# Kernel optimization log

Hardware: AMD Instinct MI355X
Metric: run time of the kernel (lower is better)

Reference implementation:

```python
import jax, jax.numpy as jnp
import numpy as np

B, T, C = 4, 2048, 1024
E, I, K = 8, 1408, 2
N_SHARED = 1
IS = I * N_SHARED  # shared expert intermediate size


def setup_inputs() -> dict:
    key = jax.random.key(0)
    ks = jax.random.split(key, 8)
    s = 0.02
    return {
        "x": jax.random.normal(ks[0], (B, T, C), dtype=jnp.float32),
        "Wg": jax.random.normal(ks[1], (E, C), dtype=jnp.float32) * s,   # gate: Linear(C->E), weight [out,in]
        "W1": jax.random.normal(ks[2], (E, I, C), dtype=jnp.float32) * s,  # fc_1 per expert
        "W2": jax.random.normal(ks[3], (E, I, C), dtype=jnp.float32) * s,  # fc_2 per expert
        "W3": jax.random.normal(ks[4], (E, C, I), dtype=jnp.float32) * s,  # proj per expert
        "Ws1": jax.random.normal(ks[5], (IS, C), dtype=jnp.float32) * s,   # shared expert fc_1
        "Ws2": jax.random.normal(ks[6], (IS, C), dtype=jnp.float32) * s,   # shared expert fc_2
        "Ws3": jax.random.normal(ks[7], (C, IS), dtype=jnp.float32) * s,   # shared expert proj
    }


def reference(x, Wg, W1, W2, W3, Ws1, Ws2, Ws3):
    b, t, c = x.shape
    xf = x.reshape(-1, c)                       # [N, C]
    n = xf.shape[0]

    # Router: softmax in float32, top-k gating
    logits = xf @ Wg.T                          # [N, E]
    probs = jax.nn.softmax(logits.astype(jnp.float32), axis=-1)
    topk_p, topk_i = jax.lax.top_k(probs, K)    # [N, K]
    topk_p = topk_p.astype(x.dtype)

    # Dense combine weights: w[n, e] = sum_k topk_p[n, k] * (topk_i[n, k] == e)
    comb = jnp.zeros((n, E), dtype=x.dtype).at[jnp.arange(n)[:, None], topk_i].add(topk_p)

    # All experts on all tokens (dense equivalent of masked dispatch), weighted combine
    g = jnp.einsum('nc,eic->nei', xf, W1)       # [N, E, I]
    u = jnp.einsum('nc,eic->nei', xf, W2)       # [N, E, I]
    h = jax.nn.silu(g) * u                      # SwiGLU
    o = jnp.einsum('nei,eci->nec', h, W3)       # [N, E, C]
    y = jnp.einsum('nec,ne->nc', o, comb).reshape(b, t, c)

    # Shared expert on the residual input
    shared = (jax.nn.silu(x @ Ws1.T) * (x @ Ws2.T)) @ Ws3.T  # [B, T, C]
    return y + shared
```

## Files before the change

kernel.cpp:

```cpp
#include <hip/hip_runtime.h>
#include <stdint.h>

typedef __bf16 bf16;
typedef __attribute__((ext_vector_type(8))) __bf16 bf16x8;
typedef __attribute__((ext_vector_type(4))) float f32x4;

#define N_TOK 8192
#define C_DIM 1024
#define I_DIM 1408
#define NE 8
#define NEA 9
#define H_ROWS 25600

#define CNT_OFF   0
#define OFFS_OFF  64
#define TT_OFF    128
#define BTOK_OFF  192
#define BP_OFF    (BTOK_OFF + NE * N_TOK * 4)
#define ROUTER_END (BP_OFF + NE * N_TOK * 4)
#define TSEL_OFF  ROUTER_END
#define TP0_OFF   (TSEL_OFF + N_TOK * 4)
#define TP1_OFF   (TP0_OFF + N_TOK * 4)
#define XB_OFF    (1u << 20)
#define WB1_OFF   (18u << 20)
#define WB2_OFF   (43u << 20)
#define WB3_OFF   (68u << 20)
#define H_OFF     (93u << 20)

__device__ __forceinline__ void gload16(const void* g, void* l) {
  __builtin_amdgcn_global_load_lds(
      (const __attribute__((address_space(1))) void*)g,
      (__attribute__((address_space(3))) void*)l, 16, 0, 0);
}

#define SCHED() __builtin_amdgcn_sched_barrier(0)
#define BAR()   __builtin_amdgcn_s_barrier()
#define VM4()   asm volatile("s_waitcnt vmcnt(4)" ::: "memory")
#define VM0()   asm volatile("s_waitcnt vmcnt(0)" ::: "memory")

#define MM(AV, BV, H)                                                          \
  {                                                                            \
    __builtin_amdgcn_s_setprio(1);                                             \
    _Pragma("unroll") for (int q = 0; q < 4; ++q)                              \
        _Pragma("unroll") for (int nf = 0; nf < 4; ++nf)                       \
            acc[(H)*4 + q][nf] = __builtin_amdgcn_mfma_f32_16x16x32_bf16(      \
                AV[q], BV[nf], acc[(H)*4 + q][nf], 0, 0, 0);                   \
    __builtin_amdgcn_s_setprio(0);                                             \
  }

__global__ __launch_bounds__(256) void convert_kernel(
    const float* __restrict__ src, bf16* __restrict__ dst, int n8) {
  int i = blockIdx.x * 256 + threadIdx.x;
  if (i >= n8) return;
  const float* s = src + (size_t)i * 8;
  float4 a = *(const float4*)(s);
  float4 b = *(const float4*)(s + 4);
  bf16x8 v;
  v[0] = (bf16)a.x; v[1] = (bf16)a.y; v[2] = (bf16)a.z; v[3] = (bf16)a.w;
  v[4] = (bf16)b.x; v[5] = (bf16)b.y; v[6] = (bf16)b.z; v[7] = (bf16)b.w;
  *(bf16x8*)(dst + (size_t)i * 8) = v;
}

__global__ __launch_bounds__(256) void logits_kernel(
    const float* __restrict__ x, const float* __restrict__ Wg,
    int* __restrict__ tsel, float* __restrict__ tp0, float* __restrict__ tp1) {
  __shared__ __align__(16) float wg[NE * C_DIM];
  int t = threadIdx.x;
#pragma unroll
  for (int j = 0; j < 8; ++j) {
    int idx = (t + 256 * j) * 4;
    *(float4*)&wg[idx] = *(const float4*)&Wg[idx];
  }
  __syncthreads();
  int wid = t >> 6, lane = t & 63;
  int tok = blockIdx.x * 4 + wid;
  const float* xr = x + (size_t)tok * C_DIM;
  float acc[NE];
#pragma unroll
  for (int e = 0; e < NE; ++e) acc[e] = 0.f;
#pragma unroll
  for (int j = 0; j < 4; ++j) {
    int c4 = (lane + 64 * j) * 4;
    float4 xv = *(const float4*)&xr[c4];
#pragma unroll
    for (int e = 0; e < NE; ++e) {
      float4 wv = *(const float4*)&wg[e * C_DIM + c4];
      acc[e] += xv.x * wv.x + xv.y * wv.y + xv.z * wv.z + xv.w * wv.w;
    }
  }
  for (int o = 32; o >= 1; o >>= 1)
#pragma unroll
    for (int e = 0; e < NE; ++e) acc[e] += __shfl_xor(acc[e], o, 64);
  if (lane == 0) {
    float m = acc[0];
#pragma unroll
    for (int e = 1; e < NE; ++e) m = fmaxf(m, acc[e]);
    float p[NE], s = 0.f;
#pragma unroll
    for (int e = 0; e < NE; ++e) { p[e] = __expf(acc[e] - m); s += p[e]; }
    float inv = 1.f / s;
#pragma unroll
    for (int e = 0; e < NE; ++e) p[e] *= inv;
    int e0 = 0; float p0 = p[0];
#pragma unroll
    for (int e = 1; e < NE; ++e) if (p[e] > p0) { p0 = p[e]; e0 = e; }
    int e1 = -1; float p1 = -1.f;
#pragma unroll
    for (int e = 0; e < NE; ++e) {
      if (e == e0) continue;
      if (p[e] > p1) { p1 = p[e]; e1 = e; }
    }
    tsel[tok] = e0 | (e1 << 8);
    tp0[tok] = p0;
    tp1[tok] = p1;
  }
}

__global__ __launch_bounds__(1024) void bucketize_kernel(
    const int* __restrict__ tsel, const float* __restrict__ tp0,
    const float* __restrict__ tp1, int* __restrict__ cnt,
    int* __restrict__ btok, float* __restrict__ bp) {
  int e = blockIdx.x;
  int t = threadIdx.x;
  __shared__ int psum[1024];
  int sel[8], loc[8];
  int cntloc = 0;
  int base_tok = t * 8;
#pragma unroll
  for (int j = 0; j < 8; ++j) {
    int s = tsel[base_tok + j];
    int hit = ((s & 0xff) == e) ? 1 : ((((s >> 8) & 0xff) == e) ? 2 : 0);
    sel[j] = hit;
    loc[j] = cntloc;
    cntloc += (hit != 0);
  }
  psum[t] = cntloc;
  __syncthreads();
  for (int off = 1; off < 1024; off <<= 1) {
    int v = (t >= off) ? psum[t - off] : 0;
    __syncthreads();
    psum[t] += v;
    __syncthreads();
  }
  int excl = psum[t] - cntloc;
  if (t == 1023) cnt[e] = psum[1023];
#pragma unroll
  for (int j = 0; j < 8; ++j) {
    if (sel[j]) {
      int pos = excl + loc[j];
      int tok = base_tok + j;
      btok[e * N_TOK + pos] = tok;
      bp[e * N_TOK + pos] = (sel[j] == 1) ? tp0[tok] : tp1[tok];
    }
  }
}

__global__ void offsets_kernel(const int* __restrict__ cnt, int* __restrict__ offs,
                               int* __restrict__ tt) {
  if (threadIdx.x == 0) {
    int a = 0, b = 0;
    for (int e = 0; e < NE; ++e) {
      offs[e] = a; tt[e] = b;
      int pad = (cnt[e] + 127) & ~127;
      a += pad;
      b += (pad + 255) >> 8;
    }
    offs[NE] = a; tt[NE] = b;
  }
}

__device__ __forceinline__ int swz_off(int row, int kg) {
  return row * 64 + ((kg ^ ((row >> 1) & 3)) * 16);
}

__global__ __launch_bounds__(512) void stage1_kernel(
    const bf16* __restrict__ xb, const bf16* __restrict__ wb1,
    const bf16* __restrict__ wb2, const int* __restrict__ cnt,
    const int* __restrict__ offs, const int* __restrict__ tt,
    const int* __restrict__ btok, bf16* __restrict__ H) {
  int bid = blockIdx.x;
  int wgid = (bid & 7) * 154 + (bid >> 3);
  int tau = wgid % 112;
  int i0 = (wgid / 112) * 128;
  int e, row0, slotbase, limit;
  if (tau < 32) {
    e = NE; row0 = tau * 256; slotbase = 0; limit = N_TOK;
  } else {
    int tr = tau - 32;
    if (tr >= tt[NE]) return;
    e = NE - 1;
#pragma unroll
    for (int q = 0; q < NE; ++q) if (tr < tt[q + 1]) { e = q; break; }
    row0 = (tr - tt[e]) * 256;
    slotbase = N_TOK + offs[e];
    limit = cnt[e];
    if (row0 >= limit) return;
  }

  __shared__ __align__(16) char smem[131072];
  const int t = threadIdx.x;
  const int lane = t & 63, wid = t >> 6;
  const int wr = wid >> 2, wc = wid & 3;
  const int l15 = lane & 15, l4 = lane >> 4;

  const int srow = t >> 2;
  const int gsrc = (t & 3) ^ ((srow >> 1) & 3);
  int ar0 = row0 + srow, ar1 = row0 + srow + 128;
  int tok0, tok1;
  if (e == NE) { tok0 = ar0; tok1 = ar1; }
  else {
    int ix0 = e * N_TOK + (ar0 < N_TOK ? ar0 : N_TOK - 1);
    int ix1 = e * N_TOK + (ar1 < N_TOK ? ar1 : N_TOK - 1);
    tok0 = btok[ix0] & (N_TOK - 1);
    tok1 = btok[ix1] & (N_TOK - 1);
  }
  const bf16* asrc0 = xb + (size_t)tok0 * C_DIM + gsrc * 8;
  const bf16* asrc1 = xb + (size_t)tok1 * C_DIM + gsrc * 8;
  const bf16* bsrc0;
  const bf16* bsrc1;
  {
    int r = srow;
    int q = r >> 4, m = q >> 1, sel = q & 1;
    int irow = i0 + m * 16 + (r & 15);
    bsrc0 = (sel ? wb2 : wb1) + ((size_t)e * I_DIM + irow) * C_DIM + gsrc * 8;
    r = srow + 128;
    q = r >> 4; m = q >> 1; sel = q & 1;
    irow = i0 + m * 16 + (r & 15);
    bsrc1 = (sel ? wb2 : wb1) + ((size_t)e * I_DIM + irow) * C_DIM + gsrc * 8;
  }
  const int lo0 = t * 16;
  const int NKT = C_DIM / 32;

  auto stAB = [&](int z) {
    if (z < NKT) {
      char* d = smem + (z & 3) * 32768;
      int k = z * 32;
      gload16(bsrc0 + k, d + 16384 + lo0);
      gload16(bsrc1 + k, d + 24576 + lo0);
      gload16(asrc0 + k, d + lo0);
      gload16(asrc1 + k, d + 8192 + lo0);
    }
  };

  int aoff[8], boff[4];
#pragma unroll
  for (int mf = 0; mf < 8; ++mf) aoff[mf] = swz_off(wr * 128 + mf * 16 + l15, l4);
#pragma unroll
  for (int nf = 0; nf < 4; ++nf) boff[nf] = swz_off(wc * 64 + nf * 16 + l15, l4);

  f32x4 acc[8][4];
  f32x4 zero = {0.f, 0.f, 0.f, 0.f};
#pragma unroll
  for (int mf = 0; mf < 8; ++mf)
#pragma unroll
    for (int nf = 0; nf < 4; ++nf) acc[mf][nf] = zero;

  bf16x8 av0[4], av1[4], bvA[4], bvB[4];
  auto rdA = [&](bf16x8* dst, int T, int h) {
    char* base = smem + (T & 3) * 32768;
#pragma unroll
    for (int q = 0; q < 4; ++q) dst[q] = *(const bf16x8*)(base + aoff[h * 4 + q]);
  };
  auto rdB = [&](bf16x8* dst, int T) {
    char* base = smem + (T & 3) * 32768 + 16384;
#pragma unroll
    for (int nf = 0; nf < 4; ++nf) dst[nf] = *(const bf16x8*)(base + boff[nf]);
  };

  stAB(0); stAB(1); stAB(2);
  SCHED(); VM4(); BAR(); SCHED();
  rdA(av0, 0, 0); rdB(bvA, 0);

  const int NIT = NKT / 2;
  for (int it = 0; it < NIT; ++it) {
    int z0 = 2 * it, z1 = 2 * it + 1;
    stAB(z0 + 3);
    rdA(av1, z0, 1);
    MM(av0, bvA, 0);
    rdA(av0, z1, 0); rdB(bvB, z1);
    MM(av1, bvA, 1);
    SCHED(); VM4(); BAR(); SCHED();
    stAB(z1 + 3);
    rdA(av1, z1, 1);
    MM(av0, bvB, 0);
    if (z1 + 1 < NKT) { rdA(av0, z1 + 1, 0); rdB(bvA, z1 + 1); }
    MM(av1, bvB, 1);
    SCHED(); VM4(); BAR(); SCHED();
  }
  VM0();

#pragma unroll
  for (int mf = 0; mf < 8; ++mf)
#pragma unroll
    for (int r = 0; r < 4; ++r) {
      int rr = row0 + wr * 128 + mf * 16 + l4 * 4 + r;
      if (rr < limit) {
#pragma unroll
        for (int p = 0; p < 2; ++p) {
          float g = acc[mf][2 * p][r];
          float u = acc[mf][2 * p + 1][r];
          float h = (g / (1.f + __expf(-g))) * u;
          int col = i0 + (wc * 2 + p) * 16 + l15;
          H[(size_t)(slotbase + rr) * I_DIM + col] = (bf16)h;
        }
      }
    }
}

template <int SHARED>
__global__ __launch_bounds__(512) void stage2_kernel(
    const bf16* __restrict__ H, const bf16* __restrict__ wb3,
    const int* __restrict__ cnt, const int* __restrict__ offs,
    const int* __restrict__ tt, const int* __restrict__ btok,
    const float* __restrict__ bp, float* __restrict__ y) {
  int bid = blockIdx.x;
  int e, row0, slotbase, limit, c0;
  if (SHARED) {
    int wgid = (bid & 7) * 16 + (bid >> 3);
    e = NE; row0 = (wgid % 32) * 256; slotbase = 0; limit = N_TOK;
    c0 = (wgid / 32) * 256;
  } else {
    int wgid = (bid & 7) * 40 + (bid >> 3);
    int tr = wgid % 80;
    c0 = (wgid / 80) * 256;
    if (tr >= tt[NE]) return;
    e = NE - 1;
#pragma unroll
    for (int q = 0; q < NE; ++q) if (tr < tt[q + 1]) { e = q; break; }
    row0 = (tr - tt[e]) * 256;
    slotbase = N_TOK + offs[e];
    limit = cnt[e];
    if (row0 >= limit) return;
  }

  __shared__ __align__(16) char smem[131072];
  const int t = threadIdx.x;
  const int lane = t & 63, wid = t >> 6;
  const int wr = wid >> 2, wc = wid & 3;
  const int l15 = lane & 15, l4 = lane >> 4;

  const int srow = t >> 2;
  const int gsrc = (t & 3) ^ ((srow >> 1) & 3);
  int sr0 = slotbase + row0 + srow;        if (sr0 > H_ROWS - 1) sr0 = H_ROWS - 1;
  int sr1 = slotbase + row0 + srow + 128;  if (sr1 > H_ROWS - 1) sr1 = H_ROWS - 1;
  const bf16* asrc0 = H + (size_t)sr0 * I_DIM + gsrc * 8;
  const bf16* asrc1 = H + (size_t)sr1 * I_DIM + gsrc * 8;
  const bf16* bsrc0 = wb3 + ((size_t)e * C_DIM + c0 + srow) * I_DIM + gsrc * 8;
  const bf16* bsrc1 = bsrc0 + (size_t)128 * I_DIM;
  const int lo0 = t * 16;
  const int NKT = I_DIM / 32;

  auto stAB = [&](int z) {
    if (z < NKT) {
      char* d = smem + (z & 3) * 32768;
      int k = z * 32;
      gload16(bsrc0 + k, d + 16384 + lo0);
      gload16(bsrc1 + k, d + 24576 + lo0);
      gload16(asrc0 + k, d + lo0);
      gload16(asrc1 + k, d + 8192 + lo0);
    }
  };

  int aoff[8], boff[4];
#pragma unroll
  for (int mf = 0; mf < 8; ++mf) aoff[mf] = swz_off(wr * 128 + mf * 16 + l15, l4);
#pragma unroll
  for (int nf = 0; nf < 4; ++nf) boff[nf] = swz_off(wc * 64 + nf * 16 + l15, l4);

  f32x4 acc[8][4];
  f32x4 zero = {0.f, 0.f, 0.f, 0.f};
#pragma unroll
  for (int mf = 0; mf < 8; ++mf)
#pragma unroll
    for (int nf = 0; nf < 4; ++nf) acc[mf][nf] = zero;

  bf16x8 av0[4], av1[4], bvA[4], bvB[4];
  auto rdA = [&](bf16x8* dst, int T, int h) {
    char* base = smem + (T & 3) * 32768;
#pragma unroll
    for (int q = 0; q < 4; ++q) dst[q] = *(const bf16x8*)(base + aoff[h * 4 + q]);
  };
  auto rdB = [&](bf16x8* dst, int T) {
    char* base = smem + (T & 3) * 32768 + 16384;
#pragma unroll
    for (int nf = 0; nf < 4; ++nf) dst[nf] = *(const bf16x8*)(base + boff[nf]);
  };

  stAB(0); stAB(1); stAB(2);
  SCHED(); VM4(); BAR(); SCHED();
  rdA(av0, 0, 0); rdB(bvA, 0);

  const int NIT = NKT / 2;
  for (int it = 0; it < NIT; ++it) {
    int z0 = 2 * it, z1 = 2 * it + 1;
    stAB(z0 + 3);
    rdA(av1, z0, 1);
    MM(av0, bvA, 0);
    rdA(av0, z1, 0); rdB(bvB, z1);
    MM(av1, bvA, 1);
    SCHED(); VM4(); BAR(); SCHED();
    stAB(z1 + 3);
    rdA(av1, z1, 1);
    MM(av0, bvB, 0);
    if (z1 + 1 < NKT) { rdA(av0, z1 + 1, 0); rdB(bvA, z1 + 1); }
    MM(av1, bvB, 1);
    SCHED(); VM4(); BAR(); SCHED();
  }
  VM0();

#pragma unroll
  for (int mf = 0; mf < 8; ++mf)
#pragma unroll
    for (int r = 0; r < 4; ++r) {
      int idx = row0 + wr * 128 + mf * 16 + l4 * 4 + r;
      if (idx < limit) {
        if (SHARED) {
#pragma unroll
          for (int nf = 0; nf < 4; ++nf) {
            int col = c0 + wc * 64 + nf * 16 + l15;
            y[(size_t)idx * C_DIM + col] = acc[mf][nf][r];
          }
        } else {
          float p = bp[e * N_TOK + idx];
          int tok = btok[e * N_TOK + idx] & (N_TOK - 1);
#pragma unroll
          for (int nf = 0; nf < 4; ++nf) {
            int col = c0 + wc * 64 + nf * 16 + l15;
            atomicAdd(&y[(size_t)tok * C_DIM + col], p * acc[mf][nf][r]);
          }
        }
      }
    }
}

extern "C" void kernel_launch(void* const* d_in, const int* in_sizes, int n_in,
                              void* d_out, int out_size, void* d_ws, size_t ws_size,
                              hipStream_t stream) {
  const float* x = (const float*)d_in[0];
  const float* Wg = (const float*)d_in[1];
  const float* W1 = (const float*)d_in[2];
  const float* W2 = (const float*)d_in[3];
  const float* W3 = (const float*)d_in[4];
  const float* Ws1 = (const float*)d_in[5];
  const float* Ws2 = (const float*)d_in[6];
  const float* Ws3 = (const float*)d_in[7];
  float* y = (float*)d_out;
  char* ws = (char*)d_ws;

  int* cnt = (int*)(ws + CNT_OFF);
  int* offs = (int*)(ws + OFFS_OFF);
  int* tt = (int*)(ws + TT_OFF);
  int* btok = (int*)(ws + BTOK_OFF);
  float* bp = (float*)(ws + BP_OFF);
  int* tsel = (int*)(ws + TSEL_OFF);
  float* tp0 = (float*)(ws + TP0_OFF);
  float* tp1 = (float*)(ws + TP1_OFF);
  bf16* xb = (bf16*)(ws + XB_OFF);
  bf16* wb1 = (bf16*)(ws + WB1_OFF);
  bf16* wb2 = (bf16*)(ws + WB2_OFF);
  bf16* wb3 = (bf16*)(ws + WB3_OFF);
  bf16* H = (bf16*)(ws + H_OFF);

  hipMemsetAsync(ws, 0, ROUTER_END, stream);

  auto conv = [&](const float* s, bf16* d, size_t n) {
    int n8 = (int)(n / 8);
    convert_kernel<<<(n8 + 255) / 256, 256, 0, stream>>>(s, d, n8);
  };
  conv(x, xb, (size_t)N_TOK * C_DIM);
  conv(W1, wb1, (size_t)NE * I_DIM * C_DIM);
  conv(Ws1, wb1 + (size_t)NE * I_DIM * C_DIM, (size_t)I_DIM * C_DIM);
  conv(W2, wb2, (size_t)NE * I_DIM * C_DIM);
  conv(Ws2, wb2 + (size_t)NE * I_DIM * C_DIM, (size_t)I_DIM * C_DIM);
  conv(W3, wb3, (size_t)NE * C_DIM * I_DIM);
  conv(Ws3, wb3 + (size_t)NE * C_DIM * I_DIM, (size_t)C_DIM * I_DIM);

  logits_kernel<<<N_TOK / 4, 256, 0, stream>>>(x, Wg, tsel, tp0, tp1);
  bucketize_kernel<<<NE, 1024, 0, stream>>>(tsel, tp0, tp1, cnt, btok, bp);
  offsets_kernel<<<1, 64, 0, stream>>>(cnt, offs, tt);

  stage1_kernel<<<1232, 512, 0, stream>>>(xb, wb1, wb2, cnt, offs, tt, btok, H);
  stage2_kernel<1><<<128, 512, 0, stream>>>(H, wb3, cnt, offs, tt, btok, bp, y);
  stage2_kernel<0><<<320, 512, 0, stream>>>(H, wb3, cnt, offs, tt, btok, bp, y);
}
```

Measured before the change: 407.4 us.

## Shrink GEMM tiles to 128x128 with 256-thread blocks and simple double buffering

Both grouped-GEMM stages move from 256x256 tiles with 512 threads and a 4-stage LDS ring to 128x128 tiles with 256 threads and a 2-stage buffer. The K loop is simplified to load, compute, then wait for all loads and barrier. Routed-expert padding granularity drops to 128 rows, which cuts wasted rows and raises block count and occupancy (launch bounds of 4 blocks). The cost is lower data reuse per tile, more global/L2 traffic, and less latency hiding from a full vmcnt(0) wait every iteration.

Measured after the change: 410.7 us. About the same (+0.8%).

```diff
diff --git a/kernel.cpp b/kernel.cpp
--- a/kernel.cpp
+++ b/kernel.cpp
@@ -35,18 +35,7 @@
 
 #define SCHED() __builtin_amdgcn_sched_barrier(0)
 #define BAR()   __builtin_amdgcn_s_barrier()
-#define VM4()   asm volatile("s_waitcnt vmcnt(4)" ::: "memory")
 #define VM0()   asm volatile("s_waitcnt vmcnt(0)" ::: "memory")
-
-#define MM(AV, BV, H)                                                          \
-  {                                                                            \
-    __builtin_amdgcn_s_setprio(1);                                             \
-    _Pragma("unroll") for (int q = 0; q < 4; ++q)                              \
-        _Pragma("unroll") for (int nf = 0; nf < 4; ++nf)                       \
-            acc[(H)*4 + q][nf] = __builtin_amdgcn_mfma_f32_16x16x32_bf16(      \
-                AV[q], BV[nf], acc[(H)*4 + q][nf], 0, 0, 0);                   \
-    __builtin_amdgcn_s_setprio(0);                                             \
-  }
 
 __global__ __launch_bounds__(256) void convert_kernel(
     const float* __restrict__ src, bf16* __restrict__ dst, int n8) {
@@ -163,7 +152,7 @@
       offs[e] = a; tt[e] = b;
       int pad = (cnt[e] + 127) & ~127;
       a += pad;
-      b += (pad + 255) >> 8;
+      b += pad >> 7;
     }
     offs[NE] = a; tt[NE] = b;
   }
@@ -173,39 +162,42 @@
   return row * 64 + ((kg ^ ((row >> 1) & 3)) * 16);
 }
 
-__global__ __launch_bounds__(512) void stage1_kernel(
+#define ROUTED_MAX 136
+#define TAU1 (64 + ROUTED_MAX)
+
+__global__ __launch_bounds__(256, 4) void stage1_kernel(
     const bf16* __restrict__ xb, const bf16* __restrict__ wb1,
     const bf16* __restrict__ wb2, const int* __restrict__ cnt,
     const int* __restrict__ offs, const int* __restrict__ tt,
     const int* __restrict__ btok, bf16* __restrict__ H) {
   int bid = blockIdx.x;
-  int wgid = (bid & 7) * 154 + (bid >> 3);
-  int tau = wgid % 112;
-  int i0 = (wgid / 112) * 128;
+  int wgid = (bid & 7) * 550 + (bid >> 3);
+  int tau = wgid % TAU1;
+  int i0 = (wgid / TAU1) * 64;
   int e, row0, slotbase, limit;
-  if (tau < 32) {
-    e = NE; row0 = tau * 256; slotbase = 0; limit = N_TOK;
+  if (tau < 64) {
+    e = NE; row0 = tau * 128; slotbase = 0; limit = N_TOK;
   } else {
-    int tr = tau - 32;
+    int tr = tau - 64;
     if (tr >= tt[NE]) return;
     e = NE - 1;
 #pragma unroll
     for (int q = 0; q < NE; ++q) if (tr < tt[q + 1]) { e = q; break; }
-    row0 = (tr - tt[e]) * 256;
+    row0 = (tr - tt[e]) * 128;
     slotbase = N_TOK + offs[e];
     limit = cnt[e];
     if (row0 >= limit) return;
   }
 
-  __shared__ __align__(16) char smem[131072];
+  __shared__ __align__(16) char smem[32768];
   const int t = threadIdx.x;
   const int lane = t & 63, wid = t >> 6;
-  const int wr = wid >> 2, wc = wid & 3;
+  const int wr = wid >> 1, wc = wid & 1;
   const int l15 = lane & 15, l4 = lane >> 4;
 
   const int srow = t >> 2;
   const int gsrc = (t & 3) ^ ((srow >> 1) & 3);
-  int ar0 = row0 + srow, ar1 = row0 + srow + 128;
+  int ar0 = row0 + srow, ar1 = row0 + srow + 64;
   int tok0, tok1;
   if (e == NE) { tok0 = ar0; tok1 = ar1; }
   else {
@@ -223,7 +215,7 @@
     int q = r >> 4, m = q >> 1, sel = q & 1;
     int irow = i0 + m * 16 + (r & 15);
     bsrc0 = (sel ? wb2 : wb1) + ((size_t)e * I_DIM + irow) * C_DIM + gsrc * 8;
-    r = srow + 128;
+    r = srow + 64;
     q = r >> 4; m = q >> 1; sel = q & 1;
     irow = i0 + m * 16 + (r & 15);
     bsrc1 = (sel ? wb2 : wb1) + ((size_t)e * I_DIM + irow) * C_DIM + gsrc * 8;
@@ -233,67 +225,54 @@
 
   auto stAB = [&](int z) {
     if (z < NKT) {
-      char* d = smem + (z & 3) * 32768;
+      char* d = smem + (z & 1) * 16384;
       int k = z * 32;
-      gload16(bsrc0 + k, d + 16384 + lo0);
-      gload16(bsrc1 + k, d + 24576 + lo0);
       gload16(asrc0 + k, d + lo0);
-      gload16(asrc1 + k, d + 8192 + lo0);
+      gload16(asrc1 + k, d + 4096 + lo0);
+      gload16(bsrc0 + k, d + 8192 + lo0);
+      gload16(bsrc1 + k, d + 12288 + lo0);
     }
   };
 
-  int aoff[8], boff[4];
-#pragma unroll
-  for (int mf = 0; mf < 8; ++mf) aoff[mf] = swz_off(wr * 128 + mf * 16 + l15, l4);
-#pragma unroll
-  for (int nf = 0; nf < 4; ++nf) boff[nf] = swz_off(wc * 64 + nf * 16 + l15, l4);
-
-  f32x4 acc[8][4];
+  int aoff[4], boff[4];
+#pragma unroll
+  for (int mf = 0; mf < 4; ++mf) aoff[mf] = swz_off(wr * 64 + mf * 16 + l15, l4);
+#pragma unroll
+  for (int nf = 0; nf < 4; ++nf) boff[nf] = 8192 + swz_off(wc * 64 + nf * 16 + l15, l4);
+
+  f32x4 acc[4][4];
   f32x4 zero = {0.f, 0.f, 0.f, 0.f};
 #pragma unroll
-  for (int mf = 0; mf < 8; ++mf)
+  for (int mf = 0; mf < 4; ++mf)
 #pragma unroll
     for (int nf = 0; nf < 4; ++nf) acc[mf][nf] = zero;
 
-  bf16x8 av0[4], av1[4], bvA[4], bvB[4];
-  auto rdA = [&](bf16x8* dst, int T, int h) {
-    char* base = smem + (T & 3) * 32768;
-#pragma unroll
-    for (int q = 0; q < 4; ++q) dst[q] = *(const bf16x8*)(base + aoff[h * 4 + q]);
-  };
-  auto rdB = [&](bf16x8* dst, int T) {
-    char* base = smem + (T & 3) * 32768 + 16384;
-#pragma unroll
-    for (int nf = 0; nf < 4; ++nf) dst[nf] = *(const bf16x8*)(base + boff[nf]);
-  };
-
-  stAB(0); stAB(1); stAB(2);
-  SCHED(); VM4(); BAR(); SCHED();
-  rdA(av0, 0, 0); rdB(bvA, 0);
-
-  const int NIT = NKT / 2;
-  for (int it = 0; it < NIT; ++it) {
-    int z0 = 2 * it, z1 = 2 * it + 1;
-    stAB(z0 + 3);
-    rdA(av1, z0, 1);
-    MM(av0, bvA, 0);
-    rdA(av0, z1, 0); rdB(bvB, z1);
-    MM(av1, bvA, 1);
-    SCHED(); VM4(); BAR(); SCHED();
-    stAB(z1 + 3);
-    rdA(av1, z1, 1);
-    MM(av0, bvB, 0);
-    if (z1 + 1 < NKT) { rdA(av0, z1 + 1, 0); rdB(bvA, z1 + 1); }
-    MM(av1, bvB, 1);
-    SCHED(); VM4(); BAR(); SCHED();
-  }
-  VM0();
-
-#pragma unroll
-  for (int mf = 0; mf < 8; ++mf)
+  stAB(0);
+  SCHED(); VM0(); BAR(); SCHED();
+
+  for (int z = 0; z < NKT; ++z) {
+    stAB(z + 1);
+    char* base = smem + (z & 1) * 16384;
+    bf16x8 av[4], bv[4];
+#pragma unroll
+    for (int mf = 0; mf < 4; ++mf) av[mf] = *(const bf16x8*)(base + aoff[mf]);
+#pragma unroll
+    for (int nf = 0; nf < 4; ++nf) bv[nf] = *(const bf16x8*)(base + boff[nf]);
+    __builtin_amdgcn_s_setprio(1);
+#pragma unroll
+    for (int mf = 0; mf < 4; ++mf)
+#pragma unroll
+      for (int nf = 0; nf < 4; ++nf)
+        acc[mf][nf] = __builtin_amdgcn_mfma_f32_16x16x32_bf16(av[mf], bv[nf], acc[mf][nf], 0, 0, 0);
+    __builtin_amdgcn_s_setprio(0);
+    SCHED(); VM0(); BAR(); SCHED();
+  }
+
+#pragma unroll
+  for (int mf = 0; mf < 4; ++mf)
 #pragma unroll
     for (int r = 0; r < 4; ++r) {
-      int rr = row0 + wr * 128 + mf * 16 + l4 * 4 + r;
+      int rr = row0 + wr * 64 + mf * 16 + l4 * 4 + r;
       if (rr < limit) {
 #pragma unroll
         for (int p = 0; p < 2; ++p) {
@@ -308,7 +287,7 @@
 }
 
 template <int SHARED>
-__global__ __launch_bounds__(512) void stage2_kernel(
+__global__ __launch_bounds__(256, 4) void stage2_kernel(
     const bf16* __restrict__ H, const bf16* __restrict__ wb3,
     const int* __restrict__ cnt, const int* __restrict__ offs,
     const int* __restrict__ tt, const int* __restrict__ btok,
@@ -316,103 +295,90 @@
   int bid = blockIdx.x;
   int e, row0, slotbase, limit, c0;
   if (SHARED) {
-    int wgid = (bid & 7) * 16 + (bid >> 3);
-    e = NE; row0 = (wgid % 32) * 256; slotbase = 0; limit = N_TOK;
-    c0 = (wgid / 32) * 256;
+    int wgid = (bid & 7) * 64 + (bid >> 3);
+    e = NE; row0 = (wgid % 64) * 128; slotbase = 0; limit = N_TOK;
+    c0 = (wgid / 64) * 128;
   } else {
-    int wgid = (bid & 7) * 40 + (bid >> 3);
-    int tr = wgid % 80;
-    c0 = (wgid / 80) * 256;
+    int wgid = (bid & 7) * 136 + (bid >> 3);
+    int tr = wgid % ROUTED_MAX;
+    c0 = (wgid / ROUTED_MAX) * 128;
     if (tr >= tt[NE]) return;
     e = NE - 1;
 #pragma unroll
     for (int q = 0; q < NE; ++q) if (tr < tt[q + 1]) { e = q; break; }
-    row0 = (tr - tt[e]) * 256;
+    row0 = (tr - tt[e]) * 128;
     slotbase = N_TOK + offs[e];
     limit = cnt[e];
     if (row0 >= limit) return;
   }
 
-  __shared__ __align__(16) char smem[131072];
+  __shared__ __align__(16) char smem[32768];
   const int t = threadIdx.x;
   const int lane = t & 63, wid = t >> 6;
-  const int wr = wid >> 2, wc = wid & 3;
+  const int wr = wid >> 1, wc = wid & 1;
   const int l15 = lane & 15, l4 = lane >> 4;
 
   const int srow = t >> 2;
   const int gsrc = (t & 3) ^ ((srow >> 1) & 3);
-  int sr0 = slotbase + row0 + srow;        if (sr0 > H_ROWS - 1) sr0 = H_ROWS - 1;
-  int sr1 = slotbase + row0 + srow + 128;  if (sr1 > H_ROWS - 1) sr1 = H_ROWS - 1;
+  int sr0 = slotbase + row0 + srow;       if (sr0 > H_ROWS - 1) sr0 = H_ROWS - 1;
+  int sr1 = slotbase + row0 + srow + 64;  if (sr1 > H_ROWS - 1) sr1 = H_ROWS - 1;
   const bf16* asrc0 = H + (size_t)sr0 * I_DIM + gsrc * 8;
   const bf16* asrc1 = H + (size_t)sr1 * I_DIM + gsrc * 8;
   const bf16* bsrc0 = wb3 + ((size_t)e * C_DIM + c0 + srow) * I_DIM + gsrc * 8;
-  const bf16* bsrc1 = bsrc0 + (size_t)128 * I_DIM;
+  const bf16* bsrc1 = bsrc0 + (size_t)64 * I_DIM;
   const int lo0 = t * 16;
   const int NKT = I_DIM / 32;
 
   auto stAB = [&](int z) {
     if (z < NKT) {
-      char* d = smem + (z & 3) * 32768;
+      char* d = smem + (z & 1) * 16384;
       int k = z * 32;
-      gload16(bsrc0 + k, d + 16384 + lo0);
-      gload16(bsrc1 + k, d + 24576 + lo0);
       gload16(asrc0 + k, d + lo0);
-      gload16(asrc1 + k, d + 8192 + lo0);
+      gload16(asrc1 + k, d + 4096 + lo0);
+      gload16(bsrc0 + k, d + 8192 + lo0);
+      gload16(bsrc1 + k, d + 12288 + lo0);
     }
   };
 
-  int aoff[8], boff[4];
-#pragma unroll
-  for (int mf = 0; mf < 8; ++mf) aoff[mf] = swz_off(wr * 128 + mf * 16 + l15, l4);
-#pragma unroll
-  for (int nf = 0; nf < 4; ++nf) boff[nf] = swz_off(wc * 64 + nf * 16 + l15, l4);
-
-  f32x4 acc[8][4];
+  int aoff[4], boff[4];
+#pragma unroll
+  for (int mf = 0; mf < 4; ++mf) aoff[mf] = swz_off(wr * 64 + mf * 16 + l15, l4);
+#pragma unroll
+  for (int nf = 0; nf < 4; ++nf) boff[nf] = 8192 + swz_off(wc * 64 + nf * 16 + l15, l4);
+
+  f32x4 acc[4][4];
   f32x4 zero = {0.f, 0.f, 0.f, 0.f};
 #pragma unroll
-  for (int mf = 0; mf < 8; ++mf)
+  for (int mf = 0; mf < 4; ++mf)
 #pragma unroll
     for (int nf = 0; nf < 4; ++nf) acc[mf][nf] = zero;
 
-  bf16x8 av0[4], av1[4], bvA[4], bvB[4];
-  auto rdA = [&](bf16x8* dst, int T, int h) {
-    char* base = smem + (T & 3) * 32768;
-#pragma unroll
-    for (int q = 0; q < 4; ++q) dst[q] = *(const bf16x8*)(base + aoff[h * 4 + q]);
-  };
-  auto rdB = [&](bf16x8* dst, int T) {
-    char* base = smem + (T & 3) * 32768 + 16384;
-#pragma unroll
-    for (int nf = 0; nf < 4; ++nf) dst[nf] = *(const bf16x8*)(base + boff[nf]);
-  };
-
-  stAB(0); stAB(1); stAB(2);
-  SCHED(); VM4(); BAR(); SCHED();
-  rdA(av0, 0, 0); rdB(bvA, 0);
-
-  const int NIT = NKT / 2;
-  for (int it = 0; it < NIT; ++it) {
-    int z0 = 2 * it, z1 = 2 * it + 1;
-    stAB(z0 + 3);
-    rdA(av1, z0, 1);
-    MM(av0, bvA, 0);
-    rdA(av0, z1, 0); rdB(bvB, z1);
-    MM(av1, bvA, 1);
-    SCHED(); VM4(); BAR(); SCHED();
-    stAB(z1 + 3);
-    rdA(av1, z1, 1);
-    MM(av0, bvB, 0);
-    if (z1 + 1 < NKT) { rdA(av0, z1 + 1, 0); rdB(bvA, z1 + 1); }
-    MM(av1, bvB, 1);
-    SCHED(); VM4(); BAR(); SCHED();
-  }
-  VM0();
-
-#pragma unroll
-  for (int mf = 0; mf < 8; ++mf)
+  stAB(0);
+  SCHED(); VM0(); BAR(); SCHED();
+
+  for (int z = 0; z < NKT; ++z) {
+    stAB(z + 1);
+    char* base = smem + (z & 1) * 16384;
+    bf16x8 av[4], bv[4];
+#pragma unroll
+    for (int mf = 0; mf < 4; ++mf) av[mf] = *(const bf16x8*)(base + aoff[mf]);
+#pragma unroll
+    for (int nf = 0; nf < 4; ++nf) bv[nf] = *(const bf16x8*)(base + boff[nf]);
+    __builtin_amdgcn_s_setprio(1);
+#pragma unroll
+    for (int mf = 0; mf < 4; ++mf)
+#pragma unroll
+      for (int nf = 0; nf < 4; ++nf)
+        acc[mf][nf] = __builtin_amdgcn_mfma_f32_16x16x32_bf16(av[mf], bv[nf], acc[mf][nf], 0, 0, 0);
+    __builtin_amdgcn_s_setprio(0);
+    SCHED(); VM0(); BAR(); SCHED();
+  }
+
+#pragma unroll
+  for (int mf = 0; mf < 4; ++mf)
 #pragma unroll
     for (int r = 0; r < 4; ++r) {
-      int idx = row0 + wr * 128 + mf * 16 + l4 * 4 + r;
+      int idx = row0 + wr * 64 + mf * 16 + l4 * 4 + r;
       if (idx < limit) {
         if (SHARED) {
 #pragma unroll
@@ -479,7 +445,7 @@
   bucketize_kernel<<<NE, 1024, 0, stream>>>(tsel, tp0, tp1, cnt, btok, bp);
   offsets_kernel<<<1, 64, 0, stream>>>(cnt, offs, tt);
 
-  stage1_kernel<<<1232, 512, 0, stream>>>(xb, wb1, wb2, cnt, offs, tt, btok, H);
-  stage2_kernel<1><<<128, 512, 0, stream>>>(H, wb3, cnt, offs, tt, btok, bp, y);
-  stage2_kernel<0><<<320, 512, 0, stream>>>(H, wb3, cnt, offs, tt, btok, bp, y);
-}
+  stage1_kernel<<<TAU1 * 22, 256, 0, stream>>>(xb, wb1, wb2, cnt, offs, tt, btok, H);
+  stage2_kernel<1><<<512, 256, 0, stream>>>(H, wb3, cnt, offs, tt, btok, bp, y);
+  stage2_kernel<0><<<ROUTED_MAX * 8, 256, 0, stream>>>(H, wb3, cnt, offs, tt, btok, bp, y);
+}
```
